# Kernel tuning notes

Measured on AMD Instinct MI355X. Metric: run time of the kernel, lower is better.

The kernel has to match this reference:

```python
import jax, jax.numpy as jnp
import numpy as np

N = 50000
E = 800000
D = 128


def setup_inputs() -> dict:
    key = jax.random.key(0)
    ks = jax.random.split(key, 6)
    x = jax.random.normal(ks[0], (N, D), dtype=jnp.float32)
    edge_index = jax.random.randint(ks[1], (2, E), 0, N, dtype=jnp.int32)
    scale = 1.0 / np.sqrt(D)
    Ws = jax.random.uniform(ks[2], (D, D), jnp.float32, -scale, scale)
    bs = jax.random.uniform(ks[3], (D,), jnp.float32, -scale, scale)
    Wn = jax.random.uniform(ks[4], (D, D), jnp.float32, -scale, scale)
    bn = jax.random.uniform(ks[5], (D,), jnp.float32, -scale, scale)
    return {"x": x, "edge_index": edge_index, "Ws": Ws, "bs": bs, "Wn": Wn, "bn": bn}


def reference(x, edge_index, Ws, bs, Wn, bn):
    # x: [N, D]; edge_index: [2, E] with rows (src, dst)
    src = edge_index[0]
    dst = edge_index[1]
    n = x.shape[0]
    # scatter-sum of gathered source features onto destinations
    agg = jax.ops.segment_sum(x[src], dst, num_segments=n)  # [N, D]
    deg = jax.ops.segment_sum(jnp.ones(dst.shape, x.dtype), dst, num_segments=n)  # [N]
    neigh = agg / jnp.clip(deg, 1.0)[:, None]  # mean aggregation, clamp deg>=1
    # torch Linear: y = x @ W.T + b
    return jax.nn.relu(x @ Ws.T + bs + neigh @ Wn.T + bn)
```

## Files before the change

kernel.cpp:

```cpp
#include <hip/hip_runtime.h>

#define D 128
#define CAP 64
#define NXCD 8
#define CHUNK 2048

typedef short bf16x8 __attribute__((ext_vector_type(8)));
typedef float f32x4 __attribute__((ext_vector_type(4)));

__device__ __forceinline__ unsigned f2bf(float f) {
    unsigned u = __builtin_bit_cast(unsigned, f);
    return (u + 0x7FFFu + ((u >> 16) & 1u)) >> 16;
}
__device__ __forceinline__ float bflo(unsigned u) {
    return __builtin_bit_cast(float, u << 16);
}
__device__ __forceinline__ float bfhi(unsigned u) {
    return __builtin_bit_cast(float, u & 0xFFFF0000u);
}

__global__ __launch_bounds__(256)
void sage_prep(const float* __restrict__ x,
               const float* __restrict__ Ws,
               const float* __restrict__ Wn,
               const int* __restrict__ ei,
               unsigned short* __restrict__ xb,
               unsigned short* __restrict__ Wsb,
               unsigned short* __restrict__ Wnb,
               unsigned short* __restrict__ srcs,
               int* __restrict__ cnt,
               int nD4, int DD4, int bucketBlocks, int E, int nodesPerXcd)
{
    const int tid = threadIdx.x;
    if ((int)blockIdx.x < bucketBlocks) {
        const int xcd = blockIdx.x & (NXCD - 1);
        const int lo = xcd * nodesPerXcd;
        const int hi = lo + nodesPerXcd;
        const int e0 = (blockIdx.x >> 3) * CHUNK + tid * 8;
        if (e0 < E) {
            const int4* sp = reinterpret_cast<const int4*>(ei + e0);
            const int4* dp = reinterpret_cast<const int4*>(ei + E + e0);
            int4 sA = sp[0], sB = sp[1];
            int4 dA = dp[0], dB = dp[1];
            int ss[8] = {sA.x, sA.y, sA.z, sA.w, sB.x, sB.y, sB.z, sB.w};
            int dd[8] = {dA.x, dA.y, dA.z, dA.w, dB.x, dB.y, dB.z, dB.w};
            #pragma unroll
            for (int q = 0; q < 8; ++q) {
                int dst = dd[q];
                if (dst >= lo && dst < hi) {
                    int pos = atomicAdd(&cnt[dst], 1);
                    if (pos < CAP) srcs[dst * CAP + pos] = (unsigned short)ss[q];
                }
            }
        }
    } else {
        int i4 = (blockIdx.x - bucketBlocks) * 256 + tid;
        const float* src; unsigned short* dst; int off;
        if (i4 < nD4)                { src = x;  dst = xb;  off = i4; }
        else if (i4 < nD4 + DD4)     { src = Ws; dst = Wsb; off = i4 - nD4; }
        else if (i4 < nD4 + 2 * DD4) { src = Wn; dst = Wnb; off = i4 - nD4 - DD4; }
        else return;
        float4 v = reinterpret_cast<const float4*>(src)[off];
        ushort4 o;
        o.x = (unsigned short)f2bf(v.x);
        o.y = (unsigned short)f2bf(v.y);
        o.z = (unsigned short)f2bf(v.z);
        o.w = (unsigned short)f2bf(v.w);
        reinterpret_cast<ushort4*>(dst)[off] = o;
    }
}

__global__ __launch_bounds__(256)
void sage_gather(const unsigned short* __restrict__ xb,
                 const unsigned short* __restrict__ srcs,
                 const int* __restrict__ cnt,
                 float* __restrict__ neighF, int n)
{
    const int lane = threadIdx.x & 63;
    const int w = threadIdx.x >> 6;
    const int tile = blockIdx.x >> 2;
    const int cg = blockIdx.x & 3;
    const int g = lane >> 3;
    const int gl = lane & 7;

    const char* xbase = (const char*)xb + cg * 64 + gl * 8;

    #pragma unroll
    for (int i = 0; i < 4; ++i) {
        const int node = tile * 16 + w * 4 + i;
        int c = cnt[node];
        c = c > CAP ? CAP : c;
        float s0 = 0.f, s1 = 0.f, s2 = 0.f, s3 = 0.f;
        if (c > 0) {
            unsigned idtab = reinterpret_cast<const unsigned*>(
                srcs + (size_t)node * CAP)[lane & 31];
            for (int kb = 0; kb < c; kb += 16) {
                #pragma unroll
                for (int q = 0; q < 2; ++q) {
                    int j = kb + q * 8 + g;
                    int jj = j < c ? j : c - 1;
                    unsigned uv = __builtin_amdgcn_ds_bpermute((jj >> 1) << 2,
                                                               (int)idtab);
                    unsigned id = (uv >> ((jj & 1) << 4)) & 0xFFFFu;
                    uint2 v = *reinterpret_cast<const uint2*>(
                        xbase + ((size_t)id << 8));
                    unsigned m = j < c ? 0xFFFFFFFFu : 0u;
                    unsigned a0 = v.x & m, a1 = v.y & m;
                    s0 += bflo(a0); s1 += bfhi(a0);
                    s2 += bflo(a1); s3 += bfhi(a1);
                }
            }
            s0 += __shfl_xor(s0, 8);  s1 += __shfl_xor(s1, 8);
            s2 += __shfl_xor(s2, 8);  s3 += __shfl_xor(s3, 8);
            s0 += __shfl_xor(s0, 16); s1 += __shfl_xor(s1, 16);
            s2 += __shfl_xor(s2, 16); s3 += __shfl_xor(s3, 16);
            s0 += __shfl_xor(s0, 32); s1 += __shfl_xor(s1, 32);
            s2 += __shfl_xor(s2, 32); s3 += __shfl_xor(s3, 32);
        }
        if (g == 0) {
            float inv = 1.f / fmaxf((float)c, 1.f);
            float4 o = {s0 * inv, s1 * inv, s2 * inv, s3 * inv};
            *reinterpret_cast<float4*>(
                neighF + (size_t)node * D + cg * 32 + gl * 4) = o;
        }
    }
}

__global__ __launch_bounds__(256)
void sage_mfma(const unsigned short* __restrict__ xb,
               const float* nF,
               const unsigned short* __restrict__ Wsb,
               const unsigned short* __restrict__ Wnb,
               const float* __restrict__ bs,
               const float* __restrict__ bn,
               float* out, int ntiles)
{
    int wave = (blockIdx.x * blockDim.x + threadIdx.x) >> 6;
    if (wave >= ntiles) return;
    int lane = threadIdx.x & 63;
    int r0 = wave * 16;
    int arow = r0 + (lane & 15);
    int kq = (lane >> 4) * 8;

    const unsigned short* xrow = xb + (size_t)arow * D + kq;
    const float* nrow = nF + (size_t)arow * D + kq;
    bf16x8 axf[4], anf[4];
#pragma unroll
    for (int ks = 0; ks < 4; ++ks) {
        axf[ks] = *reinterpret_cast<const bf16x8*>(xrow + ks * 32);
        float4 f0 = *reinterpret_cast<const float4*>(nrow + ks * 32);
        float4 f1 = *reinterpret_cast<const float4*>(nrow + ks * 32 + 4);
        bf16x8 t;
        t[0] = (short)f2bf(f0.x); t[1] = (short)f2bf(f0.y);
        t[2] = (short)f2bf(f0.z); t[3] = (short)f2bf(f0.w);
        t[4] = (short)f2bf(f1.x); t[5] = (short)f2bf(f1.y);
        t[6] = (short)f2bf(f1.z); t[7] = (short)f2bf(f1.w);
        anf[ks] = t;
    }

    const int jl = lane & 15;
    const int outrow0 = r0 + (lane >> 4) * 4;
#pragma unroll
    for (int c = 0; c < 8; ++c) {
        int j = c * 16 + jl;
        const unsigned short* wsrow = Wsb + (size_t)j * D + kq;
        const unsigned short* wnrow = Wnb + (size_t)j * D + kq;
        f32x4 acc = {0.f, 0.f, 0.f, 0.f};
#pragma unroll
        for (int ks = 0; ks < 4; ++ks) {
            bf16x8 bsf = *reinterpret_cast<const bf16x8*>(wsrow + ks * 32);
            bf16x8 bnf = *reinterpret_cast<const bf16x8*>(wnrow + ks * 32);
            acc = __builtin_amdgcn_mfma_f32_16x16x32_bf16(axf[ks], bsf, acc, 0, 0, 0);
            acc = __builtin_amdgcn_mfma_f32_16x16x32_bf16(anf[ks], bnf, acc, 0, 0, 0);
        }
        float bias = bs[j] + bn[j];
#pragma unroll
        for (int r = 0; r < 4; ++r) {
            float v = acc[r] + bias;
            out[(size_t)(outrow0 + r) * D + j] = v > 0.f ? v : 0.f;
        }
    }
}

extern "C" void kernel_launch(void* const* d_in, const int* in_sizes, int n_in,
                              void* d_out, int out_size, void* d_ws, size_t ws_size,
                              hipStream_t stream)
{
    const float* x  = (const float*)d_in[0];
    const int*   ei = (const int*)d_in[1];
    const float* Ws = (const float*)d_in[2];
    const float* bs = (const float*)d_in[3];
    const float* Wn = (const float*)d_in[4];
    const float* bn = (const float*)d_in[5];
    float* out = (float*)d_out;

    const int n = in_sizes[0] / D;
    const int E = in_sizes[1] / 2;

    unsigned short* xb   = (unsigned short*)d_ws;
    unsigned short* srcs = xb + (size_t)n * D;
    int*            cnt  = (int*)(srcs + (size_t)n * CAP);
    unsigned short* Wsb  = (unsigned short*)(cnt + n);
    unsigned short* Wnb  = Wsb + D * D;

    hipMemsetAsync(cnt, 0, (size_t)n * sizeof(int), stream);

    const int nD4 = n * D / 4;
    const int DD4 = D * D / 4;
    const int chunks       = (E + CHUNK - 1) / CHUNK;
    const int bucketBlocks = chunks * NXCD;
    const int convBlocks   = (nD4 + 2 * DD4 + 255) / 256;
    const int nodesPerXcd  = (n + NXCD - 1) / NXCD;

    sage_prep<<<bucketBlocks + convBlocks, 256, 0, stream>>>(
        x, Ws, Wn, ei, xb, Wsb, Wnb, srcs, cnt, nD4, DD4, bucketBlocks, E,
        nodesPerXcd);

    {
        int tiles = n / 16;
        sage_gather<<<tiles * 4, 256, 0, stream>>>(xb, srcs, cnt, out, n);
    }

    {
        int ntiles = n / 16;
        int blocks = (ntiles * 64 + 255) / 256;
        sage_mfma<<<blocks, 256, 0, stream>>>(xb, out, Wsb, Wnb, bs, bn,
                                              out, ntiles);
    }
}
```

Before: 211.5 us.

## Store bf16 features column-group-major so each gather block reads a compact slab

```diff
diff --git a/kernel.cpp b/kernel.cpp
--- a/kernel.cpp
+++ b/kernel.cpp
@@ -24,12 +24,13 @@
                const float* __restrict__ Ws,
                const float* __restrict__ Wn,
                const int* __restrict__ ei,
-               unsigned short* __restrict__ xb,
+               unsigned short* __restrict__ xc,
                unsigned short* __restrict__ Wsb,
                unsigned short* __restrict__ Wnb,
                unsigned short* __restrict__ srcs,
                int* __restrict__ cnt,
-               int nD4, int DD4, int bucketBlocks, int E, int nodesPerXcd)
+               int nD4, int DD4, int bucketBlocks, int E, int nodesPerXcd,
+               int n)
 {
     const int tid = threadIdx.x;
     if ((int)blockIdx.x < bucketBlocks) {
@@ -55,23 +56,33 @@
         }
     } else {
         int i4 = (blockIdx.x - bucketBlocks) * 256 + tid;
-        const float* src; unsigned short* dst; int off;
-        if (i4 < nD4)                { src = x;  dst = xb;  off = i4; }
-        else if (i4 < nD4 + DD4)     { src = Ws; dst = Wsb; off = i4 - nD4; }
-        else if (i4 < nD4 + 2 * DD4) { src = Wn; dst = Wnb; off = i4 - nD4 - DD4; }
-        else return;
+        if (i4 >= nD4 + 2 * DD4) return;
+        const float* src; int off;
+        unsigned short* dstp; int didx;
+        if (i4 < nD4) {
+            src = x; off = i4;
+            int node = i4 >> 5;
+            int fq   = i4 & 31;
+            int cg   = fq >> 3;
+            int wi   = fq & 7;
+            dstp = xc; didx = (cg * n + node) * 8 + wi;
+        } else if (i4 < nD4 + DD4) {
+            src = Ws; off = i4 - nD4; dstp = Wsb; didx = off;
+        } else {
+            src = Wn; off = i4 - nD4 - DD4; dstp = Wnb; didx = off;
+        }
         float4 v = reinterpret_cast<const float4*>(src)[off];
         ushort4 o;
         o.x = (unsigned short)f2bf(v.x);
         o.y = (unsigned short)f2bf(v.y);
         o.z = (unsigned short)f2bf(v.z);
         o.w = (unsigned short)f2bf(v.w);
-        reinterpret_cast<ushort4*>(dst)[off] = o;
+        reinterpret_cast<ushort4*>(dstp)[didx] = o;
     }
 }
 
 __global__ __launch_bounds__(256)
-void sage_gather(const unsigned short* __restrict__ xb,
+void sage_gather(const unsigned short* __restrict__ xc,
                  const unsigned short* __restrict__ srcs,
                  const int* __restrict__ cnt,
                  float* __restrict__ neighF, int n)
@@ -80,60 +91,62 @@
     const int w = threadIdx.x >> 6;
     const int tile = blockIdx.x >> 2;
     const int cg = blockIdx.x & 3;
-    const int g = lane >> 3;
-    const int gl = lane & 7;
-
-    const char* xbase = (const char*)xb + cg * 64 + gl * 8;
+    const int g = lane >> 4;
+    const int gl = lane & 15;
+
+    const char* xbase = (const char*)xc + (size_t)cg * n * 64 + gl * 4;
 
     #pragma unroll
     for (int i = 0; i < 4; ++i) {
         const int node = tile * 16 + w * 4 + i;
         int c = cnt[node];
         c = c > CAP ? CAP : c;
-        float s0 = 0.f, s1 = 0.f, s2 = 0.f, s3 = 0.f;
+        float s0 = 0.f, s1 = 0.f;
         if (c > 0) {
             unsigned idtab = reinterpret_cast<const unsigned*>(
                 srcs + (size_t)node * CAP)[lane & 31];
             for (int kb = 0; kb < c; kb += 16) {
+                unsigned v[4];
+                int jv[4];
                 #pragma unroll
-                for (int q = 0; q < 2; ++q) {
-                    int j = kb + q * 8 + g;
+                for (int q = 0; q < 4; ++q) {
+                    int j = kb + q * 4 + g;
+                    jv[q] = j;
                     int jj = j < c ? j : c - 1;
                     unsigned uv = __builtin_amdgcn_ds_bpermute((jj >> 1) << 2,
                                                                (int)idtab);
                     unsigned id = (uv >> ((jj & 1) << 4)) & 0xFFFFu;
-                    uint2 v = *reinterpret_cast<const uint2*>(
-                        xbase + ((size_t)id << 8));
-                    unsigned m = j < c ? 0xFFFFFFFFu : 0u;
-                    unsigned a0 = v.x & m, a1 = v.y & m;
-                    s0 += bflo(a0); s1 += bfhi(a0);
-                    s2 += bflo(a1); s3 += bfhi(a1);
+                    v[q] = *reinterpret_cast<const unsigned*>(
+                        xbase + ((size_t)id << 6));
+                }
+                #pragma unroll
+                for (int q = 0; q < 4; ++q) {
+                    unsigned m = jv[q] < c ? 0xFFFFFFFFu : 0u;
+                    unsigned a = v[q] & m;
+                    s0 += bflo(a);
+                    s1 += bfhi(a);
                 }
             }
-            s0 += __shfl_xor(s0, 8);  s1 += __shfl_xor(s1, 8);
-            s2 += __shfl_xor(s2, 8);  s3 += __shfl_xor(s3, 8);
             s0 += __shfl_xor(s0, 16); s1 += __shfl_xor(s1, 16);
-            s2 += __shfl_xor(s2, 16); s3 += __shfl_xor(s3, 16);
             s0 += __shfl_xor(s0, 32); s1 += __shfl_xor(s1, 32);
-            s2 += __shfl_xor(s2, 32); s3 += __shfl_xor(s3, 32);
         }
         if (g == 0) {
             float inv = 1.f / fmaxf((float)c, 1.f);
-            float4 o = {s0 * inv, s1 * inv, s2 * inv, s3 * inv};
-            *reinterpret_cast<float4*>(
-                neighF + (size_t)node * D + cg * 32 + gl * 4) = o;
+            float2 o = {s0 * inv, s1 * inv};
+            *reinterpret_cast<float2*>(
+                neighF + (size_t)node * D + cg * 32 + gl * 2) = o;
         }
     }
 }
 
 __global__ __launch_bounds__(256)
-void sage_mfma(const unsigned short* __restrict__ xb,
+void sage_mfma(const unsigned short* __restrict__ xc,
                const float* nF,
                const unsigned short* __restrict__ Wsb,
                const unsigned short* __restrict__ Wnb,
                const float* __restrict__ bs,
                const float* __restrict__ bn,
-               float* out, int ntiles)
+               float* out, int ntiles, int n)
 {
     int wave = (blockIdx.x * blockDim.x + threadIdx.x) >> 6;
     if (wave >= ntiles) return;
@@ -142,12 +155,12 @@
     int arow = r0 + (lane & 15);
     int kq = (lane >> 4) * 8;
 
-    const unsigned short* xrow = xb + (size_t)arow * D + kq;
     const float* nrow = nF + (size_t)arow * D + kq;
     bf16x8 axf[4], anf[4];
 #pragma unroll
     for (int ks = 0; ks < 4; ++ks) {
-        axf[ks] = *reinterpret_cast<const bf16x8*>(xrow + ks * 32);
+        axf[ks] = *reinterpret_cast<const bf16x8*>(
+            (const char*)xc + ((size_t)ks * n + arow) * 64 + kq * 2);
         float4 f0 = *reinterpret_cast<const float4*>(nrow + ks * 32);
         float4 f1 = *reinterpret_cast<const float4*>(nrow + ks * 32 + 4);
         bf16x8 t;
@@ -197,8 +210,8 @@
     const int n = in_sizes[0] / D;
     const int E = in_sizes[1] / 2;
 
-    unsigned short* xb   = (unsigned short*)d_ws;
-    unsigned short* srcs = xb + (size_t)n * D;
+    unsigned short* xc   = (unsigned short*)d_ws;
+    unsigned short* srcs = xc + (size_t)n * D;
     int*            cnt  = (int*)(srcs + (size_t)n * CAP);
     unsigned short* Wsb  = (unsigned short*)(cnt + n);
     unsigned short* Wnb  = Wsb + D * D;
@@ -213,18 +226,18 @@
     const int nodesPerXcd  = (n + NXCD - 1) / NXCD;
 
     sage_prep<<<bucketBlocks + convBlocks, 256, 0, stream>>>(
-        x, Ws, Wn, ei, xb, Wsb, Wnb, srcs, cnt, nD4, DD4, bucketBlocks, E,
-        nodesPerXcd);
+        x, Ws, Wn, ei, xc, Wsb, Wnb, srcs, cnt, nD4, DD4, bucketBlocks, E,
+        nodesPerXcd, n);
 
     {
         int tiles = n / 16;
-        sage_gather<<<tiles * 4, 256, 0, stream>>>(xb, srcs, cnt, out, n);
+        sage_gather<<<tiles * 4, 256, 0, stream>>>(xc, srcs, cnt, out, n);
     }
 
     {
         int ntiles = n / 16;
         int blocks = (ntiles * 64 + 255) / 256;
-        sage_mfma<<<blocks, 256, 0, stream>>>(xb, out, Wsb, Wnb, bs, bn,
-                                              out, ntiles);
-    }
-}
+        sage_mfma<<<blocks, 256, 0, stream>>>(xc, out, Wsb, Wnb, bs, bn,
+                                              out, ntiles, n);
+    }
+}
```

Result: faster. 206.0 us (-2.6%).
